# Performance work log

Measured on AMD Instinct MI355X. Metric: run time of the kernel, lower is better.

## Reference

```python
import jax, jax.numpy as jnp
import numpy as np

B, S, D = 4096, 10, 1024

def setup_inputs() -> dict:
    key = jax.random.key(0)
    ks = jax.random.split(key, 8)
    sD = 1.0 / np.sqrt(D)
    s2D = 1.0 / np.sqrt(2 * D)
    sH = 1.0 / np.sqrt(D // 2)
    return {
        "input_1": jax.random.normal(ks[0], (B, S, D), jnp.float32),
        "input_2": jax.random.normal(ks[1], (B, S, D), jnp.float32),
        # mlp_graph: Linear(2D -> D), stored (in, out)
        "Wg": jax.random.uniform(ks[2], (2 * D, D), jnp.float32, -s2D, s2D),
        "bg": jax.random.uniform(ks[3], (D,), jnp.float32, -s2D, s2D),
        # fd: Linear(2D -> D//2)
        "Wfd": jax.random.uniform(ks[4], (2 * D, D // 2), jnp.float32, -s2D, s2D),
        "bfd": jax.random.uniform(ks[5], (D // 2,), jnp.float32, -s2D, s2D),
        # ff: Linear(D//2 -> 1)
        "Wff": jax.random.uniform(ks[6], (D // 2, 1), jnp.float32, -sH, sH),
        "bff": jax.random.uniform(ks[7], (1,), jnp.float32, -sH, sH),
    }

def reference(input_1, input_2, Wg, bg, Wfd, bfd, Wff, bff):
    # graph_match: cross-graph affinity [B, S, T]
    a = jnp.einsum('bsd,btd->bst', input_1, input_2)
    a_x = jax.nn.softmax(a, axis=1)   # softmax over rows (dim=1)
    a_y = jax.nn.softmax(a, axis=0)   # unusual cross-batch softmax (dim=0)
    # attention_x = a_x^T @ input_1 ; attention_y = a_y @ input_2
    attention_x = jnp.einsum('bst,bsd->btd', a_x, input_1)
    attention_y = jnp.einsum('bst,btd->bsd', a_y, input_2)
    output_x = jnp.concatenate([input_1, attention_y], axis=2) @ Wg + bg
    output_y = jnp.concatenate([input_2, attention_x], axis=2) @ Wg + bg
    # training head: last token of each, concat, fd-ReLU-ff-Sigmoid
    o1 = output_x[:, -1, :]
    o2 = output_y[:, -1, :]
    h = jax.nn.relu(jnp.concatenate([o1, o2], axis=1) @ Wfd + bfd)
    logits = jnp.squeeze(h @ Wff + bff, axis=-1)
    return jax.nn.sigmoid(logits)
```

## Files before the change

### kernel.cpp

```cpp
#include <hip/hip_runtime.h>
#include <hip/hip_bf16.h>

#define BATCH 4096
#define SEQ 10
#define DIM 1024
#define TWOD 2048
#define HID 512

typedef __attribute__((ext_vector_type(8))) short bf16x8;
typedef __attribute__((ext_vector_type(4))) float f32x4;

#define OFF_ABF   0ull
#define OFF_OCB   (32ull << 20)
#define OFF_WGT   (48ull << 20)
#define OFF_WFDT  (52ull << 20)
#define OFF_LOG   (54ull << 20)
#define OFF_AROW  (62ull << 20)
#define OFF_STATS (OFF_AROW + 4096ull * 16 * 4)

#define GLOAD_LDS16(g, l)                                                     \
  __builtin_amdgcn_global_load_lds(                                           \
      (const __attribute__((address_space(1))) unsigned int*)(g),             \
      (__attribute__((address_space(3))) unsigned int*)(l), 16, 0, 0)

#define SW(r) (((r) + ((r) >> 2)) & 3)

static __device__ inline void store_bf4(__hip_bfloat16* p, float4 v) {
  ushort4 u;
  __hip_bfloat16 a = __float2bfloat16(v.x), b = __float2bfloat16(v.y),
                 c = __float2bfloat16(v.z), d = __float2bfloat16(v.w);
  u.x = *(unsigned short*)&a; u.y = *(unsigned short*)&b;
  u.z = *(unsigned short*)&c; u.w = *(unsigned short*)&d;
  *(ushort4*)p = u;
}

__global__ __launch_bounds__(256) void k_scores(
    const float* __restrict__ X1, const float* __restrict__ X2,
    __hip_bfloat16* __restrict__ abf, float* __restrict__ arow,
    float* __restrict__ logits) {
  int b = blockIdx.x;
  int tid = threadIdx.x;
  int wave = tid >> 6, lane = tid & 63;
  const float* x1b = X1 + (size_t)b * SEQ * DIM;
  const float* x2b = X2 + (size_t)b * SEQ * DIM;
  __shared__ float sc[20];
  __shared__ float4 xch[4 * 64];
  if (tid == 0) logits[b] = 0.f;

  const float* Abase;
  const float* Brow;
  if (wave == 0)      { Abase = x1b;           Brow = x2b + 9 * DIM; }
  else if (wave == 1) { Abase = x1b + 5 * DIM; Brow = x2b + 9 * DIM; }
  else if (wave == 2) { Abase = x2b;           Brow = x1b + 9 * DIM; }
  else                { Abase = x2b + 5 * DIM; Brow = x1b + 9 * DIM; }

  float4 ra[5][4], rb[4];
#pragma unroll
  for (int i = 0; i < 4; i++)
    rb[i] = *(const float4*)(Brow + i * 256 + lane * 4);
#pragma unroll
  for (int s = 0; s < 5; s++)
#pragma unroll
    for (int i = 0; i < 4; i++)
      ra[s][i] = *(const float4*)(Abase + s * DIM + i * 256 + lane * 4);

  float v[5];
#pragma unroll
  for (int s = 0; s < 5; s++) {
    float4 a4 = ra[s][0] * rb[0] + ra[s][1] * rb[1] + ra[s][2] * rb[2] +
                ra[s][3] * rb[3];
    v[s] = a4.x + a4.y + a4.z + a4.w;
  }
#pragma unroll
  for (int off = 1; off < 64; off <<= 1)
#pragma unroll
    for (int s = 0; s < 5; s++) v[s] += __shfl_xor(v[s], off, 64);

  if (lane == 0) {
    int base = wave * 5;
    sc[base + 0] = v[0]; sc[base + 1] = v[1]; sc[base + 2] = v[2];
    sc[base + 3] = v[3]; sc[base + 4] = v[4];
  }
  __syncthreads();

  if (tid < SEQ) arow[(size_t)b * 16 + tid] = sc[10 + tid];

  float px[SEQ];
#pragma unroll
  for (int s = 0; s < SEQ; s++) px[s] = sc[s];
  float m = -1e30f;
#pragma unroll
  for (int s = 0; s < SEQ; s++) m = fmaxf(m, px[s]);
  float w[SEQ], Z = 0.f;
#pragma unroll
  for (int s = 0; s < SEQ; s++) { w[s] = __expf(px[s] - m); Z += w[s]; }
  float inv = 1.f / Z;

  __hip_bfloat16* rowx1 = abf + (size_t)b * TWOD;
  __hip_bfloat16* rowx2 = abf + (size_t)(BATCH + b) * TWOD;

  if (wave == 1) {
#pragma unroll
    for (int i = 0; i < 4; i++) {
      float4 pb = ra[0][i] * w[5] + ra[1][i] * w[6] + ra[2][i] * w[7] +
                  ra[3][i] * w[8] + ra[4][i] * w[9];
      xch[i * 64 + lane] = pb;
      store_bf4(rowx2 + i * 256 + lane * 4, rb[i]);
    }
  } else if (wave == 2) {
#pragma unroll
    for (int i = 0; i < 4; i++)
      store_bf4(rowx1 + i * 256 + lane * 4, rb[i]);
  }
  __syncthreads();
  if (wave == 0) {
#pragma unroll
    for (int i = 0; i < 4; i++) {
      float4 ax = ra[0][i] * w[0] + ra[1][i] * w[1] + ra[2][i] * w[2] +
                  ra[3][i] * w[3] + ra[4][i] * w[4];
      ax = (ax + xch[i * 64 + lane]) * inv;
      store_bf4(rowx2 + DIM + i * 256 + lane * 4, ax);
    }
  }
}

__global__ __launch_bounds__(256) void k_stats(const float* __restrict__ arow,
                                               float* __restrict__ stats) {
  int t = blockIdx.x;
  int tid = threadIdx.x, lane = tid & 63, wave = tid >> 6;
  __shared__ float wred[4];
  float m = -1e30f;
  for (int b = tid; b < BATCH; b += 256) m = fmaxf(m, arow[(size_t)b * 16 + t]);
  for (int off = 32; off; off >>= 1) m = fmaxf(m, __shfl_down(m, off, 64));
  if (lane == 0) wred[wave] = m;
  __syncthreads();
  m = fmaxf(fmaxf(wred[0], wred[1]), fmaxf(wred[2], wred[3]));
  __syncthreads();
  float z = 0.f;
  for (int b = tid; b < BATCH; b += 256) z += __expf(arow[(size_t)b * 16 + t] - m);
  for (int off = 32; off; off >>= 1) z += __shfl_down(z, off, 64);
  if (lane == 0) wred[wave] = z;
  __syncthreads();
  if (tid == 0) {
    stats[t] = m;
    stats[16 + t] = wred[0] + wred[1] + wred[2] + wred[3];
  }
}

__global__ __launch_bounds__(256) void k_apply_y(const float* __restrict__ X2,
                                                 const float* __restrict__ arow,
                                                 const float* __restrict__ stats,
                                                 __hip_bfloat16* __restrict__ abf) {
  int b = blockIdx.x;
  int wave = threadIdx.x >> 6, lane = threadIdx.x & 63;
  float wy[SEQ];
#pragma unroll
  for (int t = 0; t < SEQ; t++)
    wy[t] = __expf(arow[(size_t)b * 16 + t] - stats[t]) / stats[16 + t];
  const float* x2b = X2 + (size_t)b * SEQ * DIM;
  int d = wave * 256 + lane * 4;
  float4 acc = {0.f, 0.f, 0.f, 0.f};
#pragma unroll
  for (int t = 0; t < SEQ; t++)
    acc += wy[t] * *(const float4*)(x2b + t * DIM + d);
  store_bf4(abf + (size_t)b * TWOD + DIM + d, acc);
}

__global__ __launch_bounds__(256) void k_transpose_both(
    const float* __restrict__ Wg, const float* __restrict__ Wfd,
    __hip_bfloat16* __restrict__ wgt, __hip_bfloat16* __restrict__ wfdt) {
  __shared__ float t[32][33];
  int by = blockIdx.y;
  const float* in;
  __hip_bfloat16* out;
  int C, c0;
  if (by < 32) { in = Wg; out = wgt; C = DIM; c0 = by * 32; }
  else         { in = Wfd; out = wfdt; C = HID; c0 = (by - 32) * 32; }
  int r0 = blockIdx.x * 32;
  int tx = threadIdx.x & 31, ty = threadIdx.x >> 5;
#pragma unroll
  for (int i = 0; i < 4; i++)
    t[ty + 8 * i][tx] = in[(size_t)(r0 + ty + 8 * i) * C + c0 + tx];
  __syncthreads();
#pragma unroll
  for (int i = 0; i < 4; i++)
    out[(size_t)(c0 + ty + 8 * i) * TWOD + r0 + tx] =
        __float2bfloat16(t[tx][ty + 8 * i]);
}

__global__ __launch_bounds__(256) void k_gemm1(
    const __hip_bfloat16* __restrict__ A, const __hip_bfloat16* __restrict__ Bt,
    const float* __restrict__ bias, __hip_bfloat16* __restrict__ outb, int K) {
  __shared__ short lds[16384];
  int tid = threadIdx.x;
  int lane = tid & 63, wave = tid >> 6;
  int flat = blockIdx.y * 8 + blockIdx.x;
  int swz = (flat & 7) * 64 + (flat >> 3);
  int m0 = (swz >> 3) * 128, n0 = (swz & 7) * 128;
  int wr = wave >> 1, wc = wave & 1;

  f32x4 acc[4][4] = {};
  int lrow = lane >> 2, ls = lane & 3;
  int g = lane >> 4, r16 = lane & 15;

  for (int k0 = 0; k0 < K; k0 += 64) {
#pragma unroll
    for (int half = 0; half < 2; half++) {
      int kk = k0 + half * 32;
#pragma unroll
      for (int c = 0; c < 2; c++) {
        int R0 = 16 * (2 * wave + c);
        int rr = R0 + lrow;
        int slot = ls ^ SW(rr);
        GLOAD_LDS16(A + (size_t)(m0 + rr) * K + kk + slot * 8,
                    &lds[half * 4096 + R0 * 32]);
        GLOAD_LDS16(Bt + (size_t)(n0 + rr) * K + kk + slot * 8,
                    &lds[8192 + half * 4096 + R0 * 32]);
      }
    }
    __syncthreads();
#pragma unroll
    for (int half = 0; half < 2; half++) {
      bf16x8 af[4], bfr[4];
#pragma unroll
      for (int mi = 0; mi < 4; mi++) {
        int m = wr * 64 + mi * 16 + r16;
        af[mi] = *(const bf16x8*)&lds[half * 4096 + m * 32 + ((g ^ SW(m)) << 3)];
      }
#pragma unroll
      for (int ni = 0; ni < 4; ni++) {
        int n = wc * 64 + ni * 16 + r16;
        bfr[ni] =
            *(const bf16x8*)&lds[8192 + half * 4096 + n * 32 + ((g ^ SW(n)) << 3)];
      }
#pragma unroll
      for (int mi = 0; mi < 4; mi++)
#pragma unroll
        for (int ni = 0; ni < 4; ni++)
          acc[mi][ni] = __builtin_amdgcn_mfma_f32_16x16x32_bf16(
              af[mi], bfr[ni], acc[mi][ni], 0, 0, 0);
    }
    __syncthreads();
  }

#pragma unroll
  for (int mi = 0; mi < 4; mi++) {
#pragma unroll
    for (int ni = 0; ni < 4; ni++) {
#pragma unroll
      for (int r = 0; r < 4; r++) {
        int m = m0 + wr * 64 + mi * 16 + g * 4 + r;
        int n = n0 + wc * 64 + ni * 16 + r16;
        float v = acc[mi][ni][r] + bias[n];
        int om = m & (BATCH - 1);
        int on = n + ((m >> 12) << 10);
        outb[(size_t)om * TWOD + on] = __float2bfloat16(v);
      }
    }
  }
}

__global__ __launch_bounds__(256) void k_gemm2_final(
    const __hip_bfloat16* __restrict__ A, const __hip_bfloat16* __restrict__ Bt,
    const float* __restrict__ bfd, const float* __restrict__ Wff,
    float* __restrict__ logits, int K) {
  __shared__ short lds[12288];
  int tid = threadIdx.x;
  int lane = tid & 63, wave = tid >> 6;
  int flat = blockIdx.y * 8 + blockIdx.x;
  int swz = (flat & 7) * 32 + (flat >> 3);
  int m0 = (swz >> 3) * 128, n0 = (swz & 7) * 64;
  int wr = wave >> 1, wc = wave & 1;

  f32x4 acc[4][2] = {};
  int lrow = lane >> 2, ls = lane & 3;
  int g = lane >> 4, r16 = lane & 15;

  for (int k0 = 0; k0 < K; k0 += 64) {
#pragma unroll
    for (int half = 0; half < 2; half++) {
      int kk = k0 + half * 32;
#pragma unroll
      for (int c = 0; c < 2; c++) {
        int R0 = 16 * (2 * wave + c);
        int rr = R0 + lrow;
        int slot = ls ^ SW(rr);
        GLOAD_LDS16(A + (size_t)(m0 + rr) * K + kk + slot * 8,
                    &lds[half * 4096 + R0 * 32]);
      }
      int RB = 16 * wave, rb = RB + lrow;
      int slotb = ls ^ SW(rb);
      GLOAD_LDS16(Bt + (size_t)(n0 + rb) * K + kk + slotb * 8,
                  &lds[8192 + half * 2048 + RB * 32]);
    }
    __syncthreads();
#pragma unroll
    for (int half = 0; half < 2; half++) {
      bf16x8 af[4], bfr[2];
#pragma unroll
      for (int mi = 0; mi < 4; mi++) {
        int m = wr * 64 + mi * 16 + r16;
        af[mi] = *(const bf16x8*)&lds[half * 4096 + m * 32 + ((g ^ SW(m)) << 3)];
      }
#pragma unroll
      for (int ni = 0; ni < 2; ni++) {
        int n = wc * 32 + ni * 16 + r16;
        bfr[ni] =
            *(const bf16x8*)&lds[8192 + half * 2048 + n * 32 + ((g ^ SW(n)) << 3)];
      }
#pragma unroll
      for (int mi = 0; mi < 4; mi++)
#pragma unroll
        for (int ni = 0; ni < 2; ni++)
          acc[mi][ni] = __builtin_amdgcn_mfma_f32_16x16x32_bf16(
              af[mi], bfr[ni], acc[mi][ni], 0, 0, 0);
    }
    __syncthreads();
  }

  int nA = n0 + wc * 32 + r16, nB = nA + 16;
  float bA = bfd[nA], bB = bfd[nB];
  float wA = Wff[nA], wB = Wff[nB];
#pragma unroll
  for (int mi = 0; mi < 4; mi++) {
#pragma unroll
    for (int r = 0; r < 4; r++) {
      float v0 = acc[mi][0][r] + bA; v0 = v0 > 0.f ? v0 : 0.f;
      float v1 = acc[mi][1][r] + bB; v1 = v1 > 0.f ? v1 : 0.f;
      float pl = v0 * wA + v1 * wB;
#pragma unroll
      for (int off = 1; off < 16; off <<= 1) pl += __shfl_xor(pl, off, 64);
      if (r16 == 0)
        atomicAdd(&logits[m0 + wr * 64 + mi * 16 + g * 4 + r], pl);
    }
  }
}

__global__ __launch_bounds__(256) void k_sigmoid(const float* __restrict__ logits,
                                                 const float* __restrict__ bff,
                                                 float* __restrict__ out) {
  int b = blockIdx.x * 256 + threadIdx.x;
  out[b] = 1.f / (1.f + __expf(-(logits[b] + bff[0])));
}

extern "C" void kernel_launch(void* const* d_in, const int* in_sizes, int n_in,
                              void* d_out, int out_size, void* d_ws, size_t ws_size,
                              hipStream_t stream) {
  const float* X1  = (const float*)d_in[0];
  const float* X2  = (const float*)d_in[1];
  const float* Wg  = (const float*)d_in[2];
  const float* bg  = (const float*)d_in[3];
  const float* Wfd = (const float*)d_in[4];
  const float* bfd = (const float*)d_in[5];
  const float* Wff = (const float*)d_in[6];
  const float* bff = (const float*)d_in[7];
  float* out = (float*)d_out;
  char* ws = (char*)d_ws;

  __hip_bfloat16* abf  = (__hip_bfloat16*)(ws + OFF_ABF);
  __hip_bfloat16* ocb  = (__hip_bfloat16*)(ws + OFF_OCB);
  __hip_bfloat16* wgt  = (__hip_bfloat16*)(ws + OFF_WGT);
  __hip_bfloat16* wfdt = (__hip_bfloat16*)(ws + OFF_WFDT);
  float* logits = (float*)(ws + OFF_LOG);
  float* arow   = (float*)(ws + OFF_AROW);
  float* stats  = (float*)(ws + OFF_STATS);

  k_transpose_both<<<dim3(64, 48), 256, 0, stream>>>(Wg, Wfd, wgt, wfdt);
  k_scores<<<BATCH, 256, 0, stream>>>(X1, X2, abf, arow, logits);
  k_stats<<<SEQ, 256, 0, stream>>>(arow, stats);
  k_apply_y<<<BATCH, 256, 0, stream>>>(X2, arow, stats, abf);
  k_gemm1<<<dim3(8, 64), 256, 0, stream>>>(abf, wgt, bg, ocb, TWOD);
  k_gemm2_final<<<dim3(8, 32), 256, 0, stream>>>(ocb, wfdt, bfd, Wff, logits,
                                                 TWOD);
  k_sigmoid<<<BATCH / 256, 256, 0, stream>>>(logits, bff, out);
}
```

Measured before the change: 194.9 us.

## Restructure gemm1 into 256x128 tiles with triple-buffered async LDS pipeline

Rewrites the first GEMM to use 512-thread blocks computing 256x128 output tiles, with a three-stage global_load_lds ring buffer so loads for tile k+2 overlap MFMA work on tile k. Explicit vmcnt waits and raw s_barrier replace the double syncthreads per iteration, and s_setprio raises priority around MFMA bursts. The aim is to hide global memory latency and cut barrier overhead in the dominant GEMM. In exchange, each block uses about 144KB of LDS, giving one block per CU, and the hardcoded 32 k-tiles assume K=2048.

```diff
diff --git a/kernel.cpp b/kernel.cpp
--- a/kernel.cpp
+++ b/kernel.cpp
@@ -188,69 +188,95 @@
         __float2bfloat16(t[tx][ty + 8 * i]);
 }
 
-__global__ __launch_bounds__(256) void k_gemm1(
+#define G1_BUF  24576
+#define G1_BOFF 16384
+#define G1_NT   32
+
+__global__ __launch_bounds__(512, 1) void k_gemm1(
     const __hip_bfloat16* __restrict__ A, const __hip_bfloat16* __restrict__ Bt,
     const float* __restrict__ bias, __hip_bfloat16* __restrict__ outb, int K) {
-  __shared__ short lds[16384];
+  __shared__ short lds[3 * G1_BUF];
   int tid = threadIdx.x;
   int lane = tid & 63, wave = tid >> 6;
-  int flat = blockIdx.y * 8 + blockIdx.x;
-  int swz = (flat & 7) * 64 + (flat >> 3);
-  int m0 = (swz >> 3) * 128, n0 = (swz & 7) * 128;
-  int wr = wave >> 1, wc = wave & 1;
-
-  f32x4 acc[4][4] = {};
-  int lrow = lane >> 2, ls = lane & 3;
+  int flat = blockIdx.x;
+  int swz = (flat & 7) * 32 + (flat >> 3);
+  int m0 = (swz >> 3) * 256, n0 = (swz & 7) * 128;
+  int wr = wave >> 2, wc = wave & 3;
   int g = lane >> 4, r16 = lane & 15;
 
-  for (int k0 = 0; k0 < K; k0 += 64) {
-#pragma unroll
-    for (int half = 0; half < 2; half++) {
-      int kk = k0 + half * 32;
-#pragma unroll
-      for (int c = 0; c < 2; c++) {
-        int R0 = 16 * (2 * wave + c);
-        int rr = R0 + lrow;
-        int slot = ls ^ SW(rr);
-        GLOAD_LDS16(A + (size_t)(m0 + rr) * K + kk + slot * 8,
-                    &lds[half * 4096 + R0 * 32]);
-        GLOAD_LDS16(Bt + (size_t)(n0 + rr) * K + kk + slot * 8,
-                    &lds[8192 + half * 4096 + R0 * 32]);
-      }
-    }
-    __syncthreads();
-#pragma unroll
-    for (int half = 0; half < 2; half++) {
-      bf16x8 af[4], bfr[4];
-#pragma unroll
-      for (int mi = 0; mi < 4; mi++) {
-        int m = wr * 64 + mi * 16 + r16;
-        af[mi] = *(const bf16x8*)&lds[half * 4096 + m * 32 + ((g ^ SW(m)) << 3)];
-      }
-#pragma unroll
-      for (int ni = 0; ni < 4; ni++) {
-        int n = wc * 64 + ni * 16 + r16;
-        bfr[ni] =
-            *(const bf16x8*)&lds[8192 + half * 4096 + n * 32 + ((g ^ SW(n)) << 3)];
-      }
-#pragma unroll
-      for (int mi = 0; mi < 4; mi++)
-#pragma unroll
-        for (int ni = 0; ni < 4; ni++)
+  int srow = tid >> 3;
+  int ss = (tid & 7) ^ (srow & 7);
+  const __hip_bfloat16* sa = A + (size_t)(m0 + srow) * K + ss * 8;
+  const __hip_bfloat16* sb = Bt + (size_t)(n0 + srow) * K + ss * 8;
+  int dA = wave * 512;
+  int dB = G1_BOFF + wave * 512;
+
+#define G1_STAGE(kt, c)                                                       \
+  {                                                                           \
+    const __hip_bfloat16* sak = sa + (kt)*64;                                 \
+    const __hip_bfloat16* sbk = sb + (kt)*64;                                 \
+    GLOAD_LDS16(sak + 0 * 64 * K, &lds[(c)*G1_BUF + dA + 0 * 4096]);          \
+    GLOAD_LDS16(sak + 1 * 64 * K, &lds[(c)*G1_BUF + dA + 1 * 4096]);          \
+    GLOAD_LDS16(sak + 2 * 64 * K, &lds[(c)*G1_BUF + dA + 2 * 4096]);          \
+    GLOAD_LDS16(sak + 3 * 64 * K, &lds[(c)*G1_BUF + dA + 3 * 4096]);          \
+    GLOAD_LDS16(sbk + 0 * 64 * K, &lds[(c)*G1_BUF + dB + 0 * 4096]);          \
+    GLOAD_LDS16(sbk + 1 * 64 * K, &lds[(c)*G1_BUF + dB + 1 * 4096]);          \
+  }
+
+  f32x4 acc[8][2] = {};
+
+  G1_STAGE(0, 0);
+  G1_STAGE(1, 1);
+  asm volatile("s_waitcnt vmcnt(6)" ::: "memory");
+  __builtin_amdgcn_sched_barrier(0);
+  __builtin_amdgcn_s_barrier();
+  __builtin_amdgcn_sched_barrier(0);
+
+#pragma unroll 1
+  for (int kt = 0; kt < G1_NT; ++kt) {
+    int cur = kt - (kt / 3) * 3;
+    if (kt + 2 < G1_NT) {
+      int nx = (kt + 2) - ((kt + 2) / 3) * 3;
+      G1_STAGE(kt + 2, nx);
+    }
+    const short* bufA = &lds[cur * G1_BUF];
+    const short* bufB = &lds[cur * G1_BUF + G1_BOFF];
+#pragma unroll
+    for (int kk = 0; kk < 2; ++kk) {
+      int sr = ((kk * 4 + g) ^ (r16 & 7)) * 8;
+      bf16x8 af[8], bfr[2];
+#pragma unroll
+      for (int mi = 0; mi < 8; mi++)
+        af[mi] = *(const bf16x8*)&bufA[(wr * 128 + mi * 16 + r16) * 64 + sr];
+#pragma unroll
+      for (int ni = 0; ni < 2; ni++)
+        bfr[ni] = *(const bf16x8*)&bufB[(wc * 32 + ni * 16 + r16) * 64 + sr];
+      __builtin_amdgcn_s_setprio(1);
+#pragma unroll
+      for (int mi = 0; mi < 8; mi++)
+#pragma unroll
+        for (int ni = 0; ni < 2; ni++)
           acc[mi][ni] = __builtin_amdgcn_mfma_f32_16x16x32_bf16(
               af[mi], bfr[ni], acc[mi][ni], 0, 0, 0);
-    }
-    __syncthreads();
-  }
-
-#pragma unroll
-  for (int mi = 0; mi < 4; mi++) {
-#pragma unroll
-    for (int ni = 0; ni < 4; ni++) {
+      __builtin_amdgcn_s_setprio(0);
+    }
+    if (kt < G1_NT - 2)
+      asm volatile("s_waitcnt vmcnt(6)" ::: "memory");
+    else
+      asm volatile("s_waitcnt vmcnt(0)" ::: "memory");
+    __builtin_amdgcn_sched_barrier(0);
+    __builtin_amdgcn_s_barrier();
+    __builtin_amdgcn_sched_barrier(0);
+  }
+
+#pragma unroll
+  for (int mi = 0; mi < 8; mi++) {
+#pragma unroll
+    for (int ni = 0; ni < 2; ni++) {
 #pragma unroll
       for (int r = 0; r < 4; r++) {
-        int m = m0 + wr * 64 + mi * 16 + g * 4 + r;
-        int n = n0 + wc * 64 + ni * 16 + r16;
+        int m = m0 + wr * 128 + mi * 16 + g * 4 + r;
+        int n = n0 + wc * 32 + ni * 16 + r16;
         float v = acc[mi][ni][r] + bias[n];
         int om = m & (BATCH - 1);
         int on = n + ((m >> 12) << 10);
@@ -258,6 +284,7 @@
       }
     }
   }
+#undef G1_STAGE
 }
 
 __global__ __launch_bounds__(256) void k_gemm2_final(
@@ -369,7 +396,7 @@
   k_scores<<<BATCH, 256, 0, stream>>>(X1, X2, abf, arow, logits);
   k_stats<<<SEQ, 256, 0, stream>>>(arow, stats);
   k_apply_y<<<BATCH, 256, 0, stream>>>(X2, arow, stats, abf);
-  k_gemm1<<<dim3(8, 64), 256, 0, stream>>>(abf, wgt, bg, ocb, TWOD);
+  k_gemm1<<<256, 512, 0, stream>>>(abf, wgt, bg, ocb, TWOD);
   k_gemm2_final<<<dim3(8, 32), 256, 0, stream>>>(ocb, wfdt, bfd, Wff, logits,
                                                  TWOD);
   k_sigmoid<<<BATCH / 256, 256, 0, stream>>>(logits, bff, out);
```

Result: faster. 182.6 us (-6.3%).
